# Kernel tuning notes

Hardware: AMD Instinct MI355X
Metric: run time of the kernel (lower is better)

The kernel has to match this reference:

```python
import jax, jax.numpy as jnp
import numpy as np

N_NODES = 100000
N_EDGES = 1600000
NFEAT = 512
NHID = 64
NCLASS = 40


def setup_inputs() -> dict:
    key = jax.random.key(0)
    ks = jax.random.split(key, 8)
    x = jax.random.normal(ks[0], (N_NODES, NFEAT), dtype=jnp.float32)
    edge_row = jax.random.randint(ks[1], (N_EDGES,), 0, N_NODES, dtype=jnp.int32)
    edge_col = jax.random.randint(ks[2], (N_EDGES,), 0, N_NODES, dtype=jnp.int32)
    # normalized adjacency values (positive, small, like D^-1/2 A D^-1/2 entries)
    adj_vals = jax.random.uniform(ks[3], (N_EDGES,), dtype=jnp.float32) * 0.1
    # Glorot-style init as in Kipf's GraphConvolution reset_parameters
    W1 = jax.random.uniform(ks[4], (NFEAT, NHID), dtype=jnp.float32,
                            minval=-1.0, maxval=1.0) / jnp.sqrt(jnp.float32(NHID))
    b1 = jax.random.uniform(ks[5], (NHID,), dtype=jnp.float32,
                            minval=-1.0, maxval=1.0) / jnp.sqrt(jnp.float32(NHID))
    W10 = jax.random.uniform(ks[6], (NHID, NCLASS), dtype=jnp.float32,
                             minval=-1.0, maxval=1.0) / jnp.sqrt(jnp.float32(NCLASS))
    b10 = jax.random.uniform(ks[7], (NCLASS,), dtype=jnp.float32,
                             minval=-1.0, maxval=1.0) / jnp.sqrt(jnp.float32(NCLASS))
    return {"x": x, "adj_vals": adj_vals, "W1": W1, "b1": b1,
            "W10": W10, "b10": b10,
            "edge_row": edge_row, "edge_col": edge_col}


def reference(x, adj_vals, W1, b1, W10, b10, edge_row, edge_col):
    def spmm(vals, feat):
        # sparse adj (COO) @ dense feat: gather source rows, scale, scatter-add to dest
        msgs = vals[:, None] * feat[edge_col]          # [E, d]
        return jax.ops.segment_sum(msgs, edge_row, num_segments=N_NODES)

    # gc1: support = x @ W1; out = spmm(adj, support) + b1
    h = spmm(adj_vals, x @ W1) + b1                    # [N, NHID]
    h = jax.nn.relu(h)
    # dropout: eval mode -> identity
    # gc10
    out = spmm(adj_vals, h @ W10) + b10                # [N, NCLASS]
    return jax.nn.log_softmax(out, axis=1)
```

## Files before the change

### kernel.cpp

```cpp
#include <hip/hip_runtime.h>

#define NND 100000
#define NE  1600000
#define NF  512
#define NH  64
#define NC  40

#define BROWS 256
#define NB ((NND + BROWS - 1) / BROWS)
#define BCAP 4864
#define EPB 8192
#define NEB ((NE + EPB - 1) / EPB)
#define W10PAD 52
#define HPAD 68

typedef unsigned short u16;
typedef unsigned int   u32;
typedef __attribute__((ext_vector_type(8))) __bf16 bf16x8;
typedef __attribute__((ext_vector_type(8))) u16    u16x8;
typedef __attribute__((ext_vector_type(4))) float  f32x4;

__device__ __forceinline__ u16 f2bf(float f) {
  u32 u = __builtin_bit_cast(u32, f);
  u += 0x7FFFu + ((u >> 16) & 1u);
  return (u16)(u >> 16);
}
__device__ __forceinline__ u32 pack2(float a, float b) {
  return (u32)f2bf(a) | ((u32)f2bf(b) << 16);
}
__device__ __forceinline__ float bf2f(u16 h) {
  return __builtin_bit_cast(float, (u32)h << 16);
}
__device__ __forceinline__ bf16x8 pack8(const float4& a, const float4& b) {
  uint4 v;
  v.x = pack2(a.x, a.y); v.y = pack2(a.z, a.w);
  v.z = pack2(b.x, b.y); v.w = pack2(b.z, b.w);
  return __builtin_bit_cast(bf16x8, v);
}

__global__ __launch_bounds__(256) void w1t_k(const float* __restrict__ W1,
                                             u16* __restrict__ w1t,
                                             int* __restrict__ gcursor) {
  if (blockIdx.x == 0) {
    for (int i = threadIdx.x; i < NB; i += 256) gcursor[i] = 0;
  }
  int i = blockIdx.x * 256 + threadIdx.x;
  if (i >= NF * NH) return;
  int n = i >> 9, k = i & 511;
  w1t[i] = f2bf(W1[(size_t)k * NH + n]);
}

__global__ __launch_bounds__(256) void gemm1_k(const float* __restrict__ x,
                                               const u16* __restrict__ w1t,
                                               u16* __restrict__ out) {
  __shared__ u16 Bs[2][64][72];
  const int t = threadIdx.x, w = t >> 6, lane = t & 63;
  const int l15 = lane & 15, l4 = lane >> 4;
  const int rowBase = blockIdx.x * 128;
  const int r0 = rowBase + w * 32 + l15;
  const float* pa0 = x + (size_t)min(r0, NND - 1) * NF + l4 * 8;
  const float* pa1 = x + (size_t)min(r0 + 16, NND - 1) * NF + l4 * 8;

  f32x4 acc[2][4];
#pragma unroll
  for (int i = 0; i < 2; ++i)
#pragma unroll
    for (int j = 0; j < 4; ++j) acc[i][j] = (f32x4){0.f, 0.f, 0.f, 0.f};

  uint4  bR[2];
  float4 aR[2][2][2];

  auto issueB = [&](int k0) {
#pragma unroll
    for (int i = 0; i < 2; ++i) {
      int c = t + i * 256;
      bR[i] = *(const uint4*)(w1t + (size_t)(c >> 3) * NF + k0 + (c & 7) * 8);
    }
  };
  auto issueA = [&](int k0) {
#pragma unroll
    for (int s = 0; s < 2; ++s) {
      const float* q0 = pa0 + k0 + s * 32;
      const float* q1 = pa1 + k0 + s * 32;
      aR[0][s][0] = *(const float4*)(q0);
      aR[0][s][1] = *(const float4*)(q0 + 4);
      aR[1][s][0] = *(const float4*)(q1);
      aR[1][s][1] = *(const float4*)(q1 + 4);
    }
  };

  issueB(0);
  issueA(0);
  for (int it = 0; it < 8; ++it) {
    const int b = it & 1;
#pragma unroll
    for (int i = 0; i < 2; ++i) {
      int c = t + i * 256;
      *(uint4*)&Bs[b][c >> 3][(c & 7) * 8] = bR[i];
    }
    bf16x8 fa0[2], fa1[2];
#pragma unroll
    for (int s = 0; s < 2; ++s) {
      fa0[s] = pack8(aR[0][s][0], aR[0][s][1]);
      fa1[s] = pack8(aR[1][s][0], aR[1][s][1]);
    }
    if (it < 7) { issueB((it + 1) * 64); issueA((it + 1) * 64); }
    __syncthreads();
#pragma unroll
    for (int s = 0; s < 2; ++s) {
#pragma unroll
      for (int ct = 0; ct < 4; ++ct) {
        bf16x8 bb = *(const bf16x8*)&Bs[b][ct * 16 + l15][s * 32 + l4 * 8];
        acc[0][ct] = __builtin_amdgcn_mfma_f32_16x16x32_bf16(fa0[s], bb, acc[0][ct], 0, 0, 0);
        acc[1][ct] = __builtin_amdgcn_mfma_f32_16x16x32_bf16(fa1[s], bb, acc[1][ct], 0, 0, 0);
      }
    }
  }

#pragma unroll
  for (int rt = 0; rt < 2; ++rt)
#pragma unroll
    for (int ct = 0; ct < 4; ++ct)
#pragma unroll
      for (int i = 0; i < 4; ++i) {
        int row = rowBase + w * 32 + rt * 16 + l4 * 4 + i;
        if (row < NND) out[(size_t)row * NH + ct * 16 + l15] = f2bf(acc[rt][ct][i]);
      }
}

__global__ __launch_bounds__(1024) void bscatter_k(const float* __restrict__ vals,
                                                   const int* __restrict__ rows,
                                                   const int* __restrict__ cols,
                                                   int* __restrict__ gcursor,
                                                   int2* __restrict__ eb1) {
  __shared__ int cnt[NB];
  __shared__ int base[NB];
  const int t = threadIdx.x;
  for (int i = t; i < NB; i += 1024) cnt[i] = 0;
  __syncthreads();
  const int gb = blockIdx.x * EPB;
  int bin[8], rnk[8], rr[8], cc[8];
  float vv[8];
#pragma unroll
  for (int k = 0; k < 8; ++k) {
    int i = gb + t + k * 1024;
    if (i < NE) {
      rr[k] = rows[i]; cc[k] = cols[i]; vv[k] = vals[i];
      bin[k] = rr[k] >> 8;
      rnk[k] = atomicAdd(&cnt[bin[k]], 1);
    } else bin[k] = -1;
  }
  __syncthreads();
  for (int i = t; i < NB; i += 1024)
    if (cnt[i]) base[i] = i * BCAP + atomicAdd(&gcursor[i], cnt[i]);
  __syncthreads();
#pragma unroll
  for (int k = 0; k < 8; ++k) {
    if (bin[k] >= 0) {
      int pos = base[bin[k]] + rnk[k];
      eb1[pos] = make_int2((int)(((u32)cc[k] << 8) | (u32)(rr[k] & 255)),
                           __float_as_int(vv[k]));
    }
  }
}

__global__ __launch_bounds__(1024) void spmm1f_k(const int* __restrict__ gcursor,
                                                 const int2* __restrict__ eb1,
                                                 const u16* __restrict__ s1,
                                                 const float* __restrict__ b1,
                                                 const float* __restrict__ W10,
                                                 u16* __restrict__ s2,
                                                 int2* __restrict__ eb2,
                                                 int* __restrict__ rowcnt) {
  __shared__ int2 se[BCAP];
  __shared__ u16 w10s[64 * W10PAD];
  __shared__ int cnt[BROWS];
  __shared__ int sc[BROWS];
  __shared__ int wsum[4];
  const int bkt = blockIdx.x, t = threadIdx.x;
  const int w = t >> 6, lane = t & 63;
  const int nE = min(gcursor[bkt], BCAP);
  const int beg = bkt * BCAP;
  for (int i = t; i < 64 * W10PAD; i += 1024) {
    int k = i / W10PAD, c = i - k * W10PAD;
    w10s[i] = (c < NC) ? f2bf(W10[k * NC + c]) : (u16)0;
  }
  if (t < BROWS) cnt[t] = 0;
  __syncthreads();
  int2 mye[5]; int myrow[5], myrank[5];
#pragma unroll
  for (int k = 0; k < 5; ++k) {
    int i = t + k * 1024;
    myrow[k] = -1;
    if (i < nE) {
      int2 e = eb1[beg + i];
      mye[k] = e;
      myrow[k] = e.x & 255;
      myrank[k] = atomicAdd(&cnt[myrow[k]], 1);
    }
  }
  __syncthreads();
  int c0 = 0, inc = 0;
  if (t < BROWS) {
    c0 = cnt[t]; inc = c0;
#pragma unroll
    for (int off = 1; off < 64; off <<= 1) {
      int u = __shfl_up(inc, off, 64);
      if ((t & 63) >= off) inc += u;
    }
    if ((t & 63) == 63) wsum[t >> 6] = inc;
  }
  __syncthreads();
  if (t < BROWS) {
    int pre = 0;
#pragma unroll
    for (int k = 0; k < 4; ++k) pre += (k < (t >> 6)) ? wsum[k] : 0;
    sc[t] = pre + inc - c0;
    rowcnt[bkt * BROWS + t] = c0;
  }
  __syncthreads();
#pragma unroll
  for (int k = 0; k < 5; ++k)
    if (myrow[k] >= 0)
      se[sc[myrow[k]] + myrank[k]] = make_int2((int)((u32)mye[k].x >> 8), mye[k].y);
  __syncthreads();

#pragma unroll
  for (int k = 0; k < 5; ++k) {
    int i = t + k * 1024;
    if (i < nE) eb2[beg + i] = se[i];
  }

  const float bias = b1[lane];
  float hreg[16];
#pragma unroll 1
  for (int i = 0; i < 16; ++i) {
    int r8 = w * 16 + i;
    int s = sc[r8], n = cnt[r8];
    float a0 = 0.f, a1 = 0.f, a2 = 0.f, a3 = 0.f;
    int j = 0;
    for (; j + 3 < n; j += 4) {
      int2 e0 = se[s + j], e1 = se[s + j + 1], e2 = se[s + j + 2], e3 = se[s + j + 3];
      a0 = fmaf(__int_as_float(e0.y), bf2f(s1[(size_t)e0.x * NH + lane]), a0);
      a1 = fmaf(__int_as_float(e1.y), bf2f(s1[(size_t)e1.x * NH + lane]), a1);
      a2 = fmaf(__int_as_float(e2.y), bf2f(s1[(size_t)e2.x * NH + lane]), a2);
      a3 = fmaf(__int_as_float(e3.y), bf2f(s1[(size_t)e3.x * NH + lane]), a3);
    }
    for (; j < n; ++j) {
      int2 e0 = se[s + j];
      a0 = fmaf(__int_as_float(e0.y), bf2f(s1[(size_t)e0.x * NH + lane]), a0);
    }
    hreg[i] = fmaxf((a0 + a1) + (a2 + a3) + bias, 0.f);
  }
  __syncthreads();

  u16* hl = (u16*)se + (size_t)w * 16 * HPAD;
#pragma unroll
  for (int i = 0; i < 16; ++i) hl[i * HPAD + lane] = f2bf(hreg[i]);

  const int l15 = lane & 15, l4 = lane >> 4;
  bf16x8 afr[2];
  afr[0] = *(const bf16x8*)&hl[l15 * HPAD + l4 * 8];
  afr[1] = *(const bf16x8*)&hl[l15 * HPAD + 32 + l4 * 8];

  f32x4 acc[3];
#pragma unroll
  for (int ct = 0; ct < 3; ++ct) acc[ct] = (f32x4){0.f, 0.f, 0.f, 0.f};
#pragma unroll
  for (int ct = 0; ct < 3; ++ct) {
#pragma unroll
    for (int kk = 0; kk < 2; ++kk) {
      u16x8 bw;
#pragma unroll
      for (int j = 0; j < 8; ++j)
        bw[j] = w10s[(kk * 32 + l4 * 8 + j) * W10PAD + ct * 16 + l15];
      acc[ct] = __builtin_amdgcn_mfma_f32_16x16x32_bf16(
          afr[kk], __builtin_bit_cast(bf16x8, bw), acc[ct], 0, 0, 0);
    }
  }
#pragma unroll
  for (int ct = 0; ct < 3; ++ct) {
    int c = ct * 16 + l15;
#pragma unroll
    for (int i = 0; i < 4; ++i) {
      int grow = bkt * BROWS + w * 16 + l4 * 4 + i;
      if (c < NC && grow < NND) s2[(size_t)grow * NC + c] = f2bf(acc[ct][i]);
    }
  }
}

__global__ __launch_bounds__(1024) void spmm2s_k(const int* __restrict__ gcursor,
                                                 const int2* __restrict__ eb2,
                                                 const int* __restrict__ rowcnt,
                                                 const u16* __restrict__ s2,
                                                 const float* __restrict__ b10,
                                                 float* __restrict__ out) {
  __shared__ int2 se[BCAP];
  __shared__ int cnt[BROWS];
  __shared__ int sc[BROWS];
  __shared__ int wsum[4];
  const int bkt = blockIdx.x, t = threadIdx.x;
  const int w = t >> 6, lane = t & 63;
  const int nE = min(gcursor[bkt], BCAP);
  const int beg = bkt * BCAP;
  if (t < BROWS) cnt[t] = rowcnt[bkt * BROWS + t];
#pragma unroll
  for (int k = 0; k < 5; ++k) {
    int i = t + k * 1024;
    if (i < nE) se[i] = eb2[beg + i];
  }
  __syncthreads();
  int c0 = 0, inc = 0;
  if (t < BROWS) {
    c0 = cnt[t]; inc = c0;
#pragma unroll
    for (int off = 1; off < 64; off <<= 1) {
      int u = __shfl_up(inc, off, 64);
      if ((t & 63) >= off) inc += u;
    }
    if ((t & 63) == 63) wsum[t >> 6] = inc;
  }
  __syncthreads();
  if (t < BROWS) {
    int pre = 0;
#pragma unroll
    for (int k = 0; k < 4; ++k) pre += (k < (t >> 6)) ? wsum[k] : 0;
    sc[t] = pre + inc - c0;
  }
  __syncthreads();

  const int off0 = (lane < NC) ? lane : 0;
  const float bias = (lane < NC) ? b10[lane] : 0.f;
#pragma unroll 1
  for (int i = 0; i < 16; ++i) {
    int r8 = w * 16 + i;
    int s = sc[r8], n = cnt[r8];
    float a0 = 0.f, a1 = 0.f, a2 = 0.f, a3 = 0.f;
    int j = 0;
    for (; j + 3 < n; j += 4) {
      int2 e0 = se[s + j], e1 = se[s + j + 1], e2 = se[s + j + 2], e3 = se[s + j + 3];
      a0 = fmaf(__int_as_float(e0.y), bf2f(s2[(size_t)e0.x * NC + off0]), a0);
      a1 = fmaf(__int_as_float(e1.y), bf2f(s2[(size_t)e1.x * NC + off0]), a1);
      a2 = fmaf(__int_as_float(e2.y), bf2f(s2[(size_t)e2.x * NC + off0]), a2);
      a3 = fmaf(__int_as_float(e3.y), bf2f(s2[(size_t)e3.x * NC + off0]), a3);
    }
    for (; j < n; ++j) {
      int2 e0 = se[s + j];
      a0 = fmaf(__int_as_float(e0.y), bf2f(s2[(size_t)e0.x * NC + off0]), a0);
    }
    int grow = bkt * BROWS + r8;
    if (grow >= NND) continue;
    float vv = (lane < NC) ? (a0 + a1) + (a2 + a3) + bias : -INFINITY;
    float m = vv;
#pragma unroll
    for (int o = 32; o; o >>= 1) m = fmaxf(m, __shfl_xor(m, o, 64));
    float e = (lane < NC) ? __expf(vv - m) : 0.f;
    float ss = e;
#pragma unroll
    for (int o = 32; o; o >>= 1) ss += __shfl_xor(ss, o, 64);
    if (lane < NC) out[(size_t)grow * NC + lane] = vv - m - __logf(ss);
  }
}

extern "C" void kernel_launch(void* const* d_in, const int* in_sizes, int n_in,
                              void* d_out, int out_size, void* d_ws, size_t ws_size,
                              hipStream_t stream) {
  const float* x    = (const float*)d_in[0];
  const float* adj  = (const float*)d_in[1];
  const float* W1   = (const float*)d_in[2];
  const float* b1   = (const float*)d_in[3];
  const float* W10  = (const float*)d_in[4];
  const float* b10  = (const float*)d_in[5];
  const int*   erow = (const int*)d_in[6];
  const int*   ecol = (const int*)d_in[7];
  float* out = (float*)d_out;

  char* p = (char*)d_ws;
  u16*  s1  = (u16*)p;    p += (size_t)NND * NH * 2;
  u16*  s2  = (u16*)p;    p += (size_t)NND * NC * 2;
  u16*  w1t = (u16*)p;    p += (size_t)NF * NH * 2;
  int2* eb1 = (int2*)p;   p += (size_t)NB * BCAP * 8;
  int2* eb2 = (int2*)p;   p += (size_t)NB * BCAP * 8;
  int* rowcnt = (int*)p;  p += (size_t)NB * BROWS * 4;
  int* gcursor = (int*)p;

  w1t_k<<<(NF * NH + 255) / 256, 256, 0, stream>>>(W1, w1t, gcursor);
  bscatter_k<<<NEB, 1024, 0, stream>>>(adj, erow, ecol, gcursor, eb1);

  gemm1_k<<<(NND + 127) / 128, 256, 0, stream>>>(x, w1t, s1);
  spmm1f_k<<<NB, 1024, 0, stream>>>(gcursor, eb1, s1, b1, W10, s2, eb2, rowcnt);
  spmm2s_k<<<NB, 1024, 0, stream>>>(gcursor, eb2, rowcnt, s2, b10, out);
}
```

Before: 198.7 us.

## Fuse edge bucketing into GEMM launch and halve bucket row count

The edge bucket-scatter and the x@W1 GEMM now share one launch. Odd blocks do the scatter and even blocks do the GEMM tile, with shared memory overlaid through a union, so the memory-bound scatter overlaps the GEMM and one launch is dropped. Buckets shrink from 256 to 128 rows and the SpMM kernels go from 1024 to 512 threads, which doubles the number of bucket blocks for better balance across CUs. The cost is more global cursor atomics and bucket entries, and a tighter per-bucket capacity margin.

```diff
diff --git a/kernel.cpp b/kernel.cpp
--- a/kernel.cpp
+++ b/kernel.cpp
@@ -6,11 +6,12 @@
 #define NH  64
 #define NC  40
 
-#define BROWS 256
+#define BROWS 128
 #define NB ((NND + BROWS - 1) / BROWS)
-#define BCAP 4864
-#define EPB 8192
-#define NEB ((NE + EPB - 1) / EPB)
+#define BCAP 2624
+#define EPB2 2048
+#define NEB2 ((NE + EPB2 - 1) / EPB2)
+#define NGT ((NND + 127) / 128)
 #define W10PAD 52
 #define HPAD 68
 
@@ -50,13 +51,54 @@
   w1t[i] = f2bf(W1[(size_t)k * NH + n]);
 }
 
-__global__ __launch_bounds__(256) void gemm1_k(const float* __restrict__ x,
-                                               const u16* __restrict__ w1t,
-                                               u16* __restrict__ out) {
-  __shared__ u16 Bs[2][64][72];
-  const int t = threadIdx.x, w = t >> 6, lane = t & 63;
+__global__ __launch_bounds__(256) void fused1_k(const float* __restrict__ x,
+                                                const u16* __restrict__ w1t,
+                                                u16* __restrict__ s1,
+                                                const float* __restrict__ vals,
+                                                const int* __restrict__ rows,
+                                                const int* __restrict__ cols,
+                                                int* __restrict__ gcursor,
+                                                int2* __restrict__ eb1) {
+  __shared__ union U {
+    struct { int cnt[NB]; int base[NB]; } sca;
+    u16 bs[2][64][72];
+  } sm;
+  const int t = threadIdx.x;
+
+  if (blockIdx.x & 1) {
+    const int cb = blockIdx.x >> 1;
+    for (int i = t; i < NB; i += 256) sm.sca.cnt[i] = 0;
+    __syncthreads();
+    const int gb = cb * EPB2;
+    int bin[8], rnk[8], rr[8], cc[8];
+    float vv[8];
+#pragma unroll
+    for (int k = 0; k < 8; ++k) {
+      int i = gb + t + k * 256;
+      if (i < NE) {
+        rr[k] = rows[i]; cc[k] = cols[i]; vv[k] = vals[i];
+        bin[k] = rr[k] >> 7;
+        rnk[k] = atomicAdd(&sm.sca.cnt[bin[k]], 1);
+      } else bin[k] = -1;
+    }
+    __syncthreads();
+    for (int i = t; i < NB; i += 256)
+      if (sm.sca.cnt[i]) sm.sca.base[i] = i * BCAP + atomicAdd(&gcursor[i], sm.sca.cnt[i]);
+    __syncthreads();
+#pragma unroll
+    for (int k = 0; k < 8; ++k) {
+      if (bin[k] >= 0) {
+        int pos = sm.sca.base[bin[k]] + rnk[k];
+        eb1[pos] = make_int2((int)(((u32)cc[k] << 7) | (u32)(rr[k] & 127)),
+                             __float_as_int(vv[k]));
+      }
+    }
+    return;
+  }
+
+  const int w = t >> 6, lane = t & 63;
   const int l15 = lane & 15, l4 = lane >> 4;
-  const int rowBase = blockIdx.x * 128;
+  const int rowBase = (blockIdx.x >> 1) * 128;
   const int r0 = rowBase + w * 32 + l15;
   const float* pa0 = x + (size_t)min(r0, NND - 1) * NF + l4 * 8;
   const float* pa1 = x + (size_t)min(r0 + 16, NND - 1) * NF + l4 * 8;
@@ -96,7 +138,7 @@
 #pragma unroll
     for (int i = 0; i < 2; ++i) {
       int c = t + i * 256;
-      *(uint4*)&Bs[b][c >> 3][(c & 7) * 8] = bR[i];
+      *(uint4*)&sm.bs[b][c >> 3][(c & 7) * 8] = bR[i];
     }
     bf16x8 fa0[2], fa1[2];
 #pragma unroll
@@ -110,7 +152,7 @@
     for (int s = 0; s < 2; ++s) {
 #pragma unroll
       for (int ct = 0; ct < 4; ++ct) {
-        bf16x8 bb = *(const bf16x8*)&Bs[b][ct * 16 + l15][s * 32 + l4 * 8];
+        bf16x8 bb = *(const bf16x8*)&sm.bs[b][ct * 16 + l15][s * 32 + l4 * 8];
         acc[0][ct] = __builtin_amdgcn_mfma_f32_16x16x32_bf16(fa0[s], bb, acc[0][ct], 0, 0, 0);
         acc[1][ct] = __builtin_amdgcn_mfma_f32_16x16x32_bf16(fa1[s], bb, acc[1][ct], 0, 0, 0);
       }
@@ -124,78 +166,42 @@
 #pragma unroll
       for (int i = 0; i < 4; ++i) {
         int row = rowBase + w * 32 + rt * 16 + l4 * 4 + i;
-        if (row < NND) out[(size_t)row * NH + ct * 16 + l15] = f2bf(acc[rt][ct][i]);
+        if (row < NND) s1[(size_t)row * NH + ct * 16 + l15] = f2bf(acc[rt][ct][i]);
       }
 }
 
-__global__ __launch_bounds__(1024) void bscatter_k(const float* __restrict__ vals,
-                                                   const int* __restrict__ rows,
-                                                   const int* __restrict__ cols,
-                                                   int* __restrict__ gcursor,
-                                                   int2* __restrict__ eb1) {
-  __shared__ int cnt[NB];
-  __shared__ int base[NB];
-  const int t = threadIdx.x;
-  for (int i = t; i < NB; i += 1024) cnt[i] = 0;
-  __syncthreads();
-  const int gb = blockIdx.x * EPB;
-  int bin[8], rnk[8], rr[8], cc[8];
-  float vv[8];
-#pragma unroll
-  for (int k = 0; k < 8; ++k) {
-    int i = gb + t + k * 1024;
-    if (i < NE) {
-      rr[k] = rows[i]; cc[k] = cols[i]; vv[k] = vals[i];
-      bin[k] = rr[k] >> 8;
-      rnk[k] = atomicAdd(&cnt[bin[k]], 1);
-    } else bin[k] = -1;
-  }
-  __syncthreads();
-  for (int i = t; i < NB; i += 1024)
-    if (cnt[i]) base[i] = i * BCAP + atomicAdd(&gcursor[i], cnt[i]);
-  __syncthreads();
-#pragma unroll
-  for (int k = 0; k < 8; ++k) {
-    if (bin[k] >= 0) {
-      int pos = base[bin[k]] + rnk[k];
-      eb1[pos] = make_int2((int)(((u32)cc[k] << 8) | (u32)(rr[k] & 255)),
-                           __float_as_int(vv[k]));
-    }
-  }
-}
-
-__global__ __launch_bounds__(1024) void spmm1f_k(const int* __restrict__ gcursor,
-                                                 const int2* __restrict__ eb1,
-                                                 const u16* __restrict__ s1,
-                                                 const float* __restrict__ b1,
-                                                 const float* __restrict__ W10,
-                                                 u16* __restrict__ s2,
-                                                 int2* __restrict__ eb2,
-                                                 int* __restrict__ rowcnt) {
+__global__ __launch_bounds__(512) void spmm1f_k(const int* __restrict__ gcursor,
+                                                const int2* __restrict__ eb1,
+                                                const u16* __restrict__ s1,
+                                                const float* __restrict__ b1,
+                                                const float* __restrict__ W10,
+                                                u16* __restrict__ s2,
+                                                int2* __restrict__ eb2,
+                                                int* __restrict__ rowcnt) {
   __shared__ int2 se[BCAP];
   __shared__ u16 w10s[64 * W10PAD];
   __shared__ int cnt[BROWS];
   __shared__ int sc[BROWS];
-  __shared__ int wsum[4];
+  __shared__ int wsum[2];
   const int bkt = blockIdx.x, t = threadIdx.x;
   const int w = t >> 6, lane = t & 63;
   const int nE = min(gcursor[bkt], BCAP);
   const int beg = bkt * BCAP;
-  for (int i = t; i < 64 * W10PAD; i += 1024) {
+  for (int i = t; i < 64 * W10PAD; i += 512) {
     int k = i / W10PAD, c = i - k * W10PAD;
     w10s[i] = (c < NC) ? f2bf(W10[k * NC + c]) : (u16)0;
   }
   if (t < BROWS) cnt[t] = 0;
   __syncthreads();
-  int2 mye[5]; int myrow[5], myrank[5];
-#pragma unroll
-  for (int k = 0; k < 5; ++k) {
-    int i = t + k * 1024;
+  int2 mye[6]; int myrow[6], myrank[6];
+#pragma unroll
+  for (int k = 0; k < 6; ++k) {
+    int i = t + k * 512;
     myrow[k] = -1;
     if (i < nE) {
       int2 e = eb1[beg + i];
       mye[k] = e;
-      myrow[k] = e.x & 255;
+      myrow[k] = e.x & 127;
       myrank[k] = atomicAdd(&cnt[myrow[k]], 1);
     }
   }
@@ -212,22 +218,20 @@
   }
   __syncthreads();
   if (t < BROWS) {
-    int pre = 0;
-#pragma unroll
-    for (int k = 0; k < 4; ++k) pre += (k < (t >> 6)) ? wsum[k] : 0;
+    int pre = (t >> 6) ? wsum[0] : 0;
     sc[t] = pre + inc - c0;
     rowcnt[bkt * BROWS + t] = c0;
   }
   __syncthreads();
 #pragma unroll
-  for (int k = 0; k < 5; ++k)
+  for (int k = 0; k < 6; ++k)
     if (myrow[k] >= 0)
-      se[sc[myrow[k]] + myrank[k]] = make_int2((int)((u32)mye[k].x >> 8), mye[k].y);
-  __syncthreads();
-
-#pragma unroll
-  for (int k = 0; k < 5; ++k) {
-    int i = t + k * 1024;
+      se[sc[myrow[k]] + myrank[k]] = make_int2((int)((u32)mye[k].x >> 7), mye[k].y);
+  __syncthreads();
+
+#pragma unroll
+  for (int k = 0; k < 6; ++k) {
+    int i = t + k * 512;
     if (i < nE) eb2[beg + i] = se[i];
   }
 
@@ -289,24 +293,24 @@
   }
 }
 
-__global__ __launch_bounds__(1024) void spmm2s_k(const int* __restrict__ gcursor,
-                                                 const int2* __restrict__ eb2,
-                                                 const int* __restrict__ rowcnt,
-                                                 const u16* __restrict__ s2,
-                                                 const float* __restrict__ b10,
-                                                 float* __restrict__ out) {
+__global__ __launch_bounds__(512) void spmm2s_k(const int* __restrict__ gcursor,
+                                                const int2* __restrict__ eb2,
+                                                const int* __restrict__ rowcnt,
+                                                const u16* __restrict__ s2,
+                                                const float* __restrict__ b10,
+                                                float* __restrict__ out) {
   __shared__ int2 se[BCAP];
   __shared__ int cnt[BROWS];
   __shared__ int sc[BROWS];
-  __shared__ int wsum[4];
+  __shared__ int wsum[2];
   const int bkt = blockIdx.x, t = threadIdx.x;
   const int w = t >> 6, lane = t & 63;
   const int nE = min(gcursor[bkt], BCAP);
   const int beg = bkt * BCAP;
   if (t < BROWS) cnt[t] = rowcnt[bkt * BROWS + t];
 #pragma unroll
-  for (int k = 0; k < 5; ++k) {
-    int i = t + k * 1024;
+  for (int k = 0; k < 6; ++k) {
+    int i = t + k * 512;
     if (i < nE) se[i] = eb2[beg + i];
   }
   __syncthreads();
@@ -322,9 +326,7 @@
   }
   __syncthreads();
   if (t < BROWS) {
-    int pre = 0;
-#pragma unroll
-    for (int k = 0; k < 4; ++k) pre += (k < (t >> 6)) ? wsum[k] : 0;
+    int pre = (t >> 6) ? wsum[0] : 0;
     sc[t] = pre + inc - c0;
   }
   __syncthreads();
@@ -385,9 +387,7 @@
   int* gcursor = (int*)p;
 
   w1t_k<<<(NF * NH + 255) / 256, 256, 0, stream>>>(W1, w1t, gcursor);
-  bscatter_k<<<NEB, 1024, 0, stream>>>(adj, erow, ecol, gcursor, eb1);
-
-  gemm1_k<<<(NND + 127) / 128, 256, 0, stream>>>(x, w1t, s1);
-  spmm1f_k<<<NB, 1024, 0, stream>>>(gcursor, eb1, s1, b1, W10, s2, eb2, rowcnt);
-  spmm2s_k<<<NB, 1024, 0, stream>>>(gcursor, eb2, rowcnt, s2, b10, out);
-}
+  fused1_k<<<NGT * 2, 256, 0, stream>>>(x, w1t, s1, adj, erow, ecol, gcursor, eb1);
+  spmm1f_k<<<NB, 512, 0, stream>>>(gcursor, eb1, s1, b1, W10, s2, eb2, rowcnt);
+  spmm2s_k<<<NB, 512, 0, stream>>>(gcursor, eb2, rowcnt, s2, b10, out);
+}
```

Result: slower. 220.7 us (+11.1%).

## Split second SpMM into half-bucket blocks using precomputed row offsets

Applied to the files above, without the earlier changes.

The first SpMM kernel now also writes absolute per-row edge offsets, so the second SpMM no longer redoes the prefix scan. The second SpMM launches two 512-thread blocks per 256-row bucket, each loading only its half of the edges into shared memory. This is meant to improve occupancy and tail balance across CUs and cut redundant scan work. The cost is an extra global array write and read.

```diff
diff --git a/kernel.cpp b/kernel.cpp
--- a/kernel.cpp
+++ b/kernel.cpp
@@ -171,6 +171,7 @@
                                                  const float* __restrict__ W10,
                                                  u16* __restrict__ s2,
                                                  int2* __restrict__ eb2,
+                                                 int* __restrict__ rowoff,
                                                  int* __restrict__ rowcnt) {
   __shared__ int2 se[BCAP];
   __shared__ u16 w10s[64 * W10PAD];
@@ -215,7 +216,9 @@
     int pre = 0;
 #pragma unroll
     for (int k = 0; k < 4; ++k) pre += (k < (t >> 6)) ? wsum[k] : 0;
-    sc[t] = pre + inc - c0;
+    int ex = pre + inc - c0;
+    sc[t] = ex;
+    rowoff[bkt * BROWS + t] = beg + ex;
     rowcnt[bkt * BROWS + t] = c0;
   }
   __syncthreads();
@@ -289,44 +292,27 @@
   }
 }
 
-__global__ __launch_bounds__(1024) void spmm2s_k(const int* __restrict__ gcursor,
-                                                 const int2* __restrict__ eb2,
-                                                 const int* __restrict__ rowcnt,
-                                                 const u16* __restrict__ s2,
-                                                 const float* __restrict__ b10,
-                                                 float* __restrict__ out) {
+__global__ __launch_bounds__(512) void spmm2h_k(const int2* __restrict__ eb2,
+                                                const int* __restrict__ rowoff,
+                                                const int* __restrict__ rowcnt,
+                                                const u16* __restrict__ s2,
+                                                const float* __restrict__ b10,
+                                                float* __restrict__ out) {
   __shared__ int2 se[BCAP];
-  __shared__ int cnt[BROWS];
-  __shared__ int sc[BROWS];
-  __shared__ int wsum[4];
-  const int bkt = blockIdx.x, t = threadIdx.x;
-  const int w = t >> 6, lane = t & 63;
-  const int nE = min(gcursor[bkt], BCAP);
-  const int beg = bkt * BCAP;
-  if (t < BROWS) cnt[t] = rowcnt[bkt * BROWS + t];
-#pragma unroll
-  for (int k = 0; k < 5; ++k) {
-    int i = t + k * 1024;
-    if (i < nE) se[i] = eb2[beg + i];
-  }
-  __syncthreads();
-  int c0 = 0, inc = 0;
-  if (t < BROWS) {
-    c0 = cnt[t]; inc = c0;
-#pragma unroll
-    for (int off = 1; off < 64; off <<= 1) {
-      int u = __shfl_up(inc, off, 64);
-      if ((t & 63) >= off) inc += u;
-    }
-    if ((t & 63) == 63) wsum[t >> 6] = inc;
-  }
-  __syncthreads();
-  if (t < BROWS) {
-    int pre = 0;
-#pragma unroll
-    for (int k = 0; k < 4; ++k) pre += (k < (t >> 6)) ? wsum[k] : 0;
-    sc[t] = pre + inc - c0;
-  }
+  __shared__ int roff[128];
+  __shared__ int rcnt[128];
+  const int bh = blockIdx.x;
+  const int bkt = bh >> 1, half = bh & 1;
+  const int t = threadIdx.x, w = t >> 6, lane = t & 63;
+  const int rowBase = bkt * BROWS + half * 128;
+  if (t < 128) {
+    roff[t] = rowoff[rowBase + t];
+    rcnt[t] = rowcnt[rowBase + t];
+  }
+  __syncthreads();
+  const int base = roff[0];
+  const int nE = min(roff[127] + rcnt[127] - base, BCAP);
+  for (int i = t; i < nE; i += 512) se[i] = eb2[base + i];
   __syncthreads();
 
   const int off0 = (lane < NC) ? lane : 0;
@@ -334,7 +320,7 @@
 #pragma unroll 1
   for (int i = 0; i < 16; ++i) {
     int r8 = w * 16 + i;
-    int s = sc[r8], n = cnt[r8];
+    int s = roff[r8] - base, n = rcnt[r8];
     float a0 = 0.f, a1 = 0.f, a2 = 0.f, a3 = 0.f;
     int j = 0;
     for (; j + 3 < n; j += 4) {
@@ -348,7 +334,7 @@
       int2 e0 = se[s + j];
       a0 = fmaf(__int_as_float(e0.y), bf2f(s2[(size_t)e0.x * NC + off0]), a0);
     }
-    int grow = bkt * BROWS + r8;
+    int grow = rowBase + r8;
     if (grow >= NND) continue;
     float vv = (lane < NC) ? (a0 + a1) + (a2 + a3) + bias : -INFINITY;
     float m = vv;
@@ -381,6 +367,7 @@
   u16*  w1t = (u16*)p;    p += (size_t)NF * NH * 2;
   int2* eb1 = (int2*)p;   p += (size_t)NB * BCAP * 8;
   int2* eb2 = (int2*)p;   p += (size_t)NB * BCAP * 8;
+  int* rowoff = (int*)p;  p += (size_t)NB * BROWS * 4;
   int* rowcnt = (int*)p;  p += (size_t)NB * BROWS * 4;
   int* gcursor = (int*)p;
 
@@ -388,6 +375,6 @@
   bscatter_k<<<NEB, 1024, 0, stream>>>(adj, erow, ecol, gcursor, eb1);
 
   gemm1_k<<<(NND + 127) / 128, 256, 0, stream>>>(x, w1t, s1);
-  spmm1f_k<<<NB, 1024, 0, stream>>>(gcursor, eb1, s1, b1, W10, s2, eb2, rowcnt);
-  spmm2s_k<<<NB, 1024, 0, stream>>>(gcursor, eb2, rowcnt, s2, b10, out);
-}
+  spmm1f_k<<<NB, 1024, 0, stream>>>(gcursor, eb1, s1, b1, W10, s2, eb2, rowoff, rowcnt);
+  spmm2h_k<<<NB * 2, 512, 0, stream>>>(eb2, rowoff, rowcnt, s2, b10, out);
+}
```

Result: no change. 196.1 us (-1.3%).
